# Optimization experiments

Measured on AMD Instinct MI355X. Metric: run time of the kernel, lower is better.

## Reference

```python
import jax, jax.numpy as jnp
import numpy as np


def setup_inputs() -> dict:
    key = jax.random.key(0)
    k1, k2 = jax.random.split(key)
    B, H, W = 8, 720, 1280
    input1 = jax.random.normal(k1, (B, 2, H, W), dtype=jnp.float32)   # flow (fx, fy)
    input2 = jax.random.uniform(k2, (B, 1, H, W), dtype=jnp.float32)  # depth weight > 0
    return {"input1": input1, "input2": input2}


def _depth_flow_projection(flow, depth):
    # flow:  [B, 2, H, W]; depth: [B, 1, H, W]
    # Faithful to DAIN's DepthFlowProjection CUDA kernel with fillhole=0
    # (requires_grad=True path): each source pixel splats -flow * depth to the
    # 4 integer neighbors of its projected location, count accumulates depth
    # at the same 4 neighbors, then output /= count where count > 0.
    B, _, H, W = flow.shape
    fx = flow[:, 0]           # [B, H, W]
    fy = flow[:, 1]
    d = depth[:, 0]

    jj = jnp.arange(W, dtype=flow.dtype)[None, None, :]
    ii = jnp.arange(H, dtype=flow.dtype)[None, :, None]
    x2 = jj + fx              # projected x, [B, H, W]
    y2 = ii + fy              # projected y

    valid = (x2 >= 0) & (x2 <= W - 1) & (y2 >= 0) & (y2 <= H - 1)
    w = jnp.where(valid, d, 0.0)  # zero weight kills out-of-bounds splats

    xL = jnp.clip(jnp.floor(x2), 0, W - 1).astype(jnp.int32)
    yT = jnp.clip(jnp.floor(y2), 0, H - 1).astype(jnp.int32)
    xR = jnp.minimum(xL + 1, W - 1)
    yB = jnp.minimum(yT + 1, H - 1)

    boff = (jnp.arange(B, dtype=jnp.int32) * (H * W))[:, None, None]
    # flat indices for the 4 corners, each [B*H*W]
    corners = [(yT, xL), (yT, xR), (yB, xL), (yB, xR)]
    idx = jnp.stack([(boff + yy * W + xx).reshape(-1) for yy, xx in corners], 0).reshape(-1)  # [4*B*H*W]

    def rep4(v):
        v = v.reshape(-1)
        return jnp.broadcast_to(v[None, :], (4, v.shape[0])).reshape(-1)

    N = B * H * W
    count = jnp.zeros((N,), flow.dtype).at[idx].add(rep4(w))
    ox = jnp.zeros((N,), flow.dtype).at[idx].add(rep4(-fx * w))
    oy = jnp.zeros((N,), flow.dtype).at[idx].add(rep4(-fy * w))

    has = count > 0
    denom = jnp.where(has, count, 1.0)
    ox = jnp.where(has, ox / denom, 0.0)
    oy = jnp.where(has, oy / denom, 0.0)
    return jnp.stack([ox.reshape(B, H, W), oy.reshape(B, H, W)], axis=1)  # [B, 2, H, W]


def reference(input1, input2):
    return _depth_flow_projection(input1, input2)
```

## Files before the change

### kernel.cpp

```cpp
#include <hip/hip_runtime.h>

constexpr int B  = 8;
constexpr int H  = 720;
constexpr int W  = 1280;
constexpr int HW = H * W;
constexpr int N  = B * HW;

constexpr int TX = 64;
constexpr int TY = 16;
constexpr int C  = 3;
constexpr int RW = TX + 2 * C;
constexpr int RH = TY + 2 * C;
constexpr int RN = RW * RH;
constexpr int PY = 4;

__global__ __launch_bounds__(256) void dfp_zero(float* __restrict__ p)
{
    size_t t = ((size_t)blockIdx.x * 256 + threadIdx.x) * 4;
    *(float4*)(p + t) = make_float4(0.f, 0.f, 0.f, 0.f);
}

__global__ __launch_bounds__(256) void dfp_outlier(
    const float* __restrict__ flow, const float* __restrict__ depth,
    float* __restrict__ pcnt, float* __restrict__ pox, float* __restrict__ poy)
{
    int t = blockIdx.x * 256 + threadIdx.x;
    if (t >= N / 4) return;
    int t4 = t * 4;
    int b  = t4 / HW;
    int p  = t4 - b * HW;
    int i  = p / W;
    int j  = p - i * W;

    const float* fxp = flow + b * 2 * HW;
    float4 fx4 = *(const float4*)(fxp + p);
    float4 fy4 = *(const float4*)(fxp + HW + p);
    float fxs[4] = {fx4.x, fx4.y, fx4.z, fx4.w};
    float fys[4] = {fy4.x, fy4.y, fy4.z, fy4.w};

    float* cb = pcnt + b * HW;
    float* xb = pox  + b * HW;
    float* yb = poy  + b * HW;

    #pragma unroll
    for (int e = 0; e < 4; ++e) {
        float fx = fxs[e], fy = fys[e];
        float x2 = (float)(j + e) + fx;
        float y2 = (float)i + fy;
        bool valid = (x2 >= 0.0f) && (x2 <= (float)(W - 1)) &&
                     (y2 >= 0.0f) && (y2 <= (float)(H - 1));
        bool band  = (fx >= -3.0f) && (fx < 3.0f) &&
                     (fy >= -3.0f) && (fy < 3.0f);
        bool fast  = band && (x2 < (float)(W - 1)) && (y2 < (float)(H - 1));
        if (valid && !fast) {
            float d  = depth[t4 + e];
            int xL = (int)floorf(x2);
            int yT = (int)floorf(y2);
            int xR = min(xL + 1, W - 1);
            int yB = min(yT + 1, H - 1);
            float w = d, gx = -fx * d, gy = -fy * d;
            int n00 = yT * W + xL, n01 = yT * W + xR;
            int n10 = yB * W + xL, n11 = yB * W + xR;
            unsafeAtomicAdd(&cb[n00], w); unsafeAtomicAdd(&xb[n00], gx); unsafeAtomicAdd(&yb[n00], gy);
            unsafeAtomicAdd(&cb[n01], w); unsafeAtomicAdd(&xb[n01], gx); unsafeAtomicAdd(&yb[n01], gy);
            unsafeAtomicAdd(&cb[n10], w); unsafeAtomicAdd(&xb[n10], gx); unsafeAtomicAdd(&yb[n10], gy);
            unsafeAtomicAdd(&cb[n11], w); unsafeAtomicAdd(&xb[n11], gx); unsafeAtomicAdd(&yb[n11], gy);
        }
    }
}

__global__ __launch_bounds__(256) void dfp_gather(
    const float* __restrict__ flow, const float* __restrict__ depth,
    const float* __restrict__ pcnt, const float* __restrict__ pox,
    const float* __restrict__ poy, float* __restrict__ out)
{
    __shared__ float4 sq[RN];

    const int tid = threadIdx.x;
    const int tx0 = blockIdx.x * TX;
    const int ty0 = blockIdx.y * TY;
    const int b   = blockIdx.z;

    const float* fxp = flow + b * 2 * HW;
    const float* fyp = fxp + HW;
    const float* dp  = depth + b * HW;

    for (int k = tid; k < RN; k += 256) {
        int ry = k / RW;
        int rx = k - ry * RW;
        int gy = ty0 - C + ry;
        int gx = tx0 - C + rx;
        float X = 0.f, Y = 0.f, w = 0.f;
        if ((unsigned)gy < (unsigned)H && (unsigned)gx < (unsigned)W) {
            int g = gy * W + gx;
            float fx = fxp[g];
            float fy = fyp[g];
            float x2 = (float)gx + fx;
            float y2 = (float)gy + fy;
            if (fx >= -3.0f && fx < 3.0f && fy >= -3.0f && fy < 3.0f &&
                x2 >= 0.0f && x2 < (float)(W - 1) &&
                y2 >= 0.0f && y2 < (float)(H - 1)) {
                X = x2; Y = y2; w = dp[g];
            }
        }
        sq[k] = make_float4(X, Y, w, 0.f);
    }
    __syncthreads();

    const int ox  = tid & 63;
    const int g0  = tid >> 6;
    const int oxa = tx0 + ox;

    const float oxaF = (float)oxa;
    const float cLo  = oxaF - 1.0f;
    const float cHi  = oxaF + 1.0f;

    const int oy0 = g0 * PY;
    const int oyb = ty0 + oy0;
    const float oybF = (float)oyb;
    const float bm1 = oybF - 1.0f;
    const float b0  = oybF;
    const float b1  = oybF + 1.0f;
    const float b2  = oybF + 2.0f;
    const float b3  = oybF + 3.0f;
    const float b4  = oybF + 4.0f;

    float c0 = 0.f, c1 = 0.f, c2 = 0.f, c3 = 0.f;
    float x0 = 0.f, x1 = 0.f, x2a = 0.f, x3 = 0.f;
    float y0 = 0.f, y1 = 0.f, y2a = 0.f, y3 = 0.f;

    for (int dy = -C; dy <= PY - 1 + C; ++dy) {
        const int   base = (oy0 + dy + C) * RW + ox;
        const float gyF  = oybF + (float)dy;
        #pragma unroll
        for (int dx = -C; dx <= C; ++dx) {
            float4 f = sq[base + dx + C];
            const float X = f.x, Y = f.y, w = f.z;
            bool cx  = (X >= cLo) & (X < cHi);
            bool tm1 = (Y >= bm1);
            bool t0  = (Y >= b0);
            bool t1  = (Y >= b1);
            bool t2  = (Y >= b2);
            bool t3  = (Y >= b3);
            bool t4  = (Y >= b4);
            bool m0 = cx & tm1 & !t1;
            bool m1 = cx & t0  & !t2;
            bool m2 = cx & t1  & !t3;
            bool m3 = cx & t2  & !t4;

            float ax = (oxaF + (float)dx) - X;
            float ay = gyF - Y;

            float w0 = m0 ? w : 0.0f;
            float w1 = m1 ? w : 0.0f;
            float w2 = m2 ? w : 0.0f;
            float w3 = m3 ? w : 0.0f;
            c0 += w0;  x0  = fmaf(ax, w0, x0 );  y0  = fmaf(ay, w0, y0 );
            c1 += w1;  x1  = fmaf(ax, w1, x1 );  y1  = fmaf(ay, w1, y1 );
            c2 += w2;  x2a = fmaf(ax, w2, x2a);  y2a = fmaf(ay, w2, y2a);
            c3 += w3;  x3  = fmaf(ax, w3, x3 );  y3  = fmaf(ay, w3, y3 );
        }
    }

    float* outx = out + b * 2 * HW;
    float* outy = outx + HW;
    const float* cb = pcnt + b * HW;
    const float* xb = pox  + b * HW;
    const float* yb = poy  + b * HW;

    float cc[PY] = {c0, c1, c2, c3};
    float vx[PY] = {x0, x1, x2a, x3};
    float vy[PY] = {y0, y1, y2a, y3};
    #pragma unroll
    for (int r = 0; r < PY; ++r) {
        int ga = (oyb + r) * W + oxa;
        float c  = cc[r] + cb[ga];
        float fx = vx[r] + xb[ga];
        float fy = vy[r] + yb[ga];
        bool has = c > 0.0f;
        outx[ga] = has ? fx / c : 0.0f;
        outy[ga] = has ? fy / c : 0.0f;
    }
}

__global__ __launch_bounds__(256) void dfp_scatter(
    const float* __restrict__ flow, const float* __restrict__ depth,
    float* __restrict__ out, float* __restrict__ count)
{
    int t = blockIdx.x * 256 + threadIdx.x;
    if (t >= N) return;
    int b = t / HW;
    int p = t - b * HW;
    int i = p / W;
    int j = p - i * W;
    const int fbase = b * 2 * HW;
    float fx = flow[fbase + p];
    float fy = flow[fbase + HW + p];
    float d  = depth[t];
    float x2 = (float)j + fx;
    float y2 = (float)i + fy;
    if (!(x2 >= 0.0f && x2 <= (float)(W - 1) &&
          y2 >= 0.0f && y2 <= (float)(H - 1))) return;
    int xL = (int)floorf(x2);
    int yT = (int)floorf(y2);
    int xR = min(xL + 1, W - 1);
    int yB = min(yT + 1, H - 1);
    float w = d, gx = -fx * w, gy = -fy * w;
    float* ox = out + fbase;
    float* oy = out + fbase + HW;
    float* cnt = count + b * HW;
    int n00 = yT * W + xL, n01 = yT * W + xR, n10 = yB * W + xL, n11 = yB * W + xR;
    unsafeAtomicAdd(&cnt[n00], w); unsafeAtomicAdd(&ox[n00], gx); unsafeAtomicAdd(&oy[n00], gy);
    unsafeAtomicAdd(&cnt[n01], w); unsafeAtomicAdd(&ox[n01], gx); unsafeAtomicAdd(&oy[n01], gy);
    unsafeAtomicAdd(&cnt[n10], w); unsafeAtomicAdd(&ox[n10], gx); unsafeAtomicAdd(&oy[n10], gy);
    unsafeAtomicAdd(&cnt[n11], w); unsafeAtomicAdd(&ox[n11], gx); unsafeAtomicAdd(&oy[n11], gy);
}

__global__ __launch_bounds__(256) void dfp_normalize(
    float* __restrict__ out, const float* __restrict__ count)
{
    int t = blockIdx.x * 256 + threadIdx.x;
    if (t >= N / 4) return;
    int t4 = t * 4;
    int b  = t4 / HW;
    int p  = t4 - b * HW;
    float4 c = *(const float4*)(count + t4);
    float* ox = out + b * 2 * HW + p;
    float* oy = ox + HW;
    float4 vx = *(const float4*)ox;
    float4 vy = *(const float4*)oy;
    vx.x = (c.x > 0.0f) ? vx.x / c.x : 0.0f;
    vx.y = (c.y > 0.0f) ? vx.y / c.y : 0.0f;
    vx.z = (c.z > 0.0f) ? vx.z / c.z : 0.0f;
    vx.w = (c.w > 0.0f) ? vx.w / c.w : 0.0f;
    vy.x = (c.x > 0.0f) ? vy.x / c.x : 0.0f;
    vy.y = (c.y > 0.0f) ? vy.y / c.y : 0.0f;
    vy.z = (c.z > 0.0f) ? vy.z / c.z : 0.0f;
    vy.w = (c.w > 0.0f) ? vy.w / c.w : 0.0f;
    *(float4*)ox = vx;
    *(float4*)oy = vy;
}

extern "C" void kernel_launch(void* const* d_in, const int* in_sizes, int n_in,
                              void* d_out, int out_size, void* d_ws, size_t ws_size,
                              hipStream_t stream)
{
    const float* flow  = (const float*)d_in[0];
    const float* depth = (const float*)d_in[1];
    float* out = (float*)d_out;

    if (ws_size >= (size_t)3 * N * sizeof(float)) {
        float* pcnt = (float*)d_ws;
        float* pox  = pcnt + N;
        float* poy  = pox + N;
        dfp_zero<<<(3 * N / 4) / 256, 256, 0, stream>>>(pcnt);
        dfp_outlier<<<(N / 4 + 255) / 256, 256, 0, stream>>>(flow, depth, pcnt, pox, poy);
        dim3 grid(W / TX, H / TY, B);
        dfp_gather<<<grid, 256, 0, stream>>>(flow, depth, pcnt, pox, poy, out);
    } else if (ws_size >= (size_t)N * sizeof(float)) {
        float* count = (float*)d_ws;
        hipMemsetAsync(out,   0, (size_t)2 * N * sizeof(float), stream);
        hipMemsetAsync(count, 0, (size_t)N * sizeof(float),     stream);
        dfp_scatter  <<<(N + 255) / 256,     256, 0, stream>>>(flow, depth, out, count);
        dfp_normalize<<<(N / 4 + 255) / 256, 256, 0, stream>>>(out, count);
    }
}
```

Before: 248.4 us.

## Register-block gather kernel to 2x3 outputs per thread with parity-split shared tile

The gather kernel now computes a 2-column by 3-row block of output pixels per thread instead of a 1x4 column strip, using a 128x12 tile. The shared tile is stored with even and odd columns split into separate halves, so each loaded candidate is reused across two output columns without bank conflicts. Final loads and stores become float2. The aim is fewer shared-memory loads per output and better amortized comparisons; the cost is more accumulator registers, hence the added occupancy hint in launch bounds.

Result: slower. 280.0 us (+12.7%).

```diff
diff --git a/kernel.cpp b/kernel.cpp
--- a/kernel.cpp
+++ b/kernel.cpp
@@ -6,13 +6,12 @@
 constexpr int HW = H * W;
 constexpr int N  = B * HW;
 
-constexpr int TX = 64;
-constexpr int TY = 16;
-constexpr int C  = 3;
-constexpr int RW = TX + 2 * C;
-constexpr int RH = TY + 2 * C;
-constexpr int RN = RW * RH;
-constexpr int PY = 4;
+constexpr int TX  = 128;
+constexpr int TY  = 12;
+constexpr int C   = 3;
+constexpr int RWS = TX + 2 * C;
+constexpr int RHS = TY + 2 * C;
+constexpr int RNS = RWS * RHS;
 
 __global__ __launch_bounds__(256) void dfp_zero(float* __restrict__ p)
 {
@@ -69,12 +68,12 @@
     }
 }
 
-__global__ __launch_bounds__(256) void dfp_gather(
+__global__ __launch_bounds__(256, 4) void dfp_gather(
     const float* __restrict__ flow, const float* __restrict__ depth,
     const float* __restrict__ pcnt, const float* __restrict__ pox,
     const float* __restrict__ poy, float* __restrict__ out)
 {
-    __shared__ float4 sq[RN];
+    __shared__ float4 sq[RNS];
 
     const int tid = threadIdx.x;
     const int tx0 = blockIdx.x * TX;
@@ -85,11 +84,11 @@
     const float* fyp = fxp + HW;
     const float* dp  = depth + b * HW;
 
-    for (int k = tid; k < RN; k += 256) {
-        int ry = k / RW;
-        int rx = k - ry * RW;
+    for (int k = tid; k < RNS; k += 256) {
+        int ry = k / RWS;
+        int s  = k - ry * RWS;
         int gy = ty0 - C + ry;
-        int gx = tx0 - C + rx;
+        int gx = tx0 - C + s;
         float X = 0.f, Y = 0.f, w = 0.f;
         if ((unsigned)gy < (unsigned)H && (unsigned)gx < (unsigned)W) {
             int g = gy * W + gx;
@@ -103,62 +102,77 @@
                 X = x2; Y = y2; w = dp[g];
             }
         }
-        sq[k] = make_float4(X, Y, w, 0.f);
+        int idx = ry * RWS + (s & 1) * (RWS / 2) + (s >> 1);
+        sq[idx] = make_float4(X, Y, w, 0.f);
     }
     __syncthreads();
 
-    const int ox  = tid & 63;
-    const int g0  = tid >> 6;
-    const int oxa = tx0 + ox;
-
-    const float oxaF = (float)oxa;
-    const float cLo  = oxaF - 1.0f;
-    const float cHi  = oxaF + 1.0f;
-
-    const int oy0 = g0 * PY;
-    const int oyb = ty0 + oy0;
+    const int cg   = tid & 63;
+    const int rg   = tid >> 6;
+    const int oxa0 = tx0 + 2 * cg;
+
+    const float oxaF = (float)oxa0;
+    const float cm1 = oxaF - 1.0f;
+    const float cc0 = oxaF;
+    const float cp1 = oxaF + 1.0f;
+    const float cp2 = oxaF + 2.0f;
+
+    const int oyb = ty0 + rg * 3;
     const float oybF = (float)oyb;
     const float bm1 = oybF - 1.0f;
-    const float b0  = oybF;
-    const float b1  = oybF + 1.0f;
-    const float b2  = oybF + 2.0f;
-    const float b3  = oybF + 3.0f;
-    const float b4  = oybF + 4.0f;
-
-    float c0 = 0.f, c1 = 0.f, c2 = 0.f, c3 = 0.f;
-    float x0 = 0.f, x1 = 0.f, x2a = 0.f, x3 = 0.f;
-    float y0 = 0.f, y1 = 0.f, y2a = 0.f, y3 = 0.f;
-
-    for (int dy = -C; dy <= PY - 1 + C; ++dy) {
-        const int   base = (oy0 + dy + C) * RW + ox;
-        const float gyF  = oybF + (float)dy;
+    const float b0_ = oybF;
+    const float b1_ = oybF + 1.0f;
+    const float b2_ = oybF + 2.0f;
+    const float b3_ = oybF + 3.0f;
+
+    float c00=0.f,c01=0.f,c02=0.f, c10=0.f,c11=0.f,c12=0.f;
+    float x00=0.f,x01=0.f,x02=0.f, x10=0.f,x11=0.f,x12=0.f;
+    float y00=0.f,y01=0.f,y02=0.f, y10=0.f,y11=0.f,y12=0.f;
+
+    for (int dy = -C; dy <= 2 + C; ++dy) {
+        const int   rb  = (rg * 3 + dy + C) * RWS;
+        const int   be  = rb + cg;
+        const int   bo  = rb + (RWS / 2) + cg;
+        const float gyF = oybF + (float)dy;
+
         #pragma unroll
-        for (int dx = -C; dx <= C; ++dx) {
-            float4 f = sq[base + dx + C];
-            const float X = f.x, Y = f.y, w = f.z;
-            bool cx  = (X >= cLo) & (X < cHi);
-            bool tm1 = (Y >= bm1);
-            bool t0  = (Y >= b0);
-            bool t1  = (Y >= b1);
-            bool t2  = (Y >= b2);
-            bool t3  = (Y >= b3);
-            bool t4  = (Y >= b4);
-            bool m0 = cx & tm1 & !t1;
-            bool m1 = cx & t0  & !t2;
-            bool m2 = cx & t1  & !t3;
-            bool m3 = cx & t2  & !t4;
-
-            float ax = (oxaF + (float)dx) - X;
-            float ay = gyF - Y;
-
-            float w0 = m0 ? w : 0.0f;
-            float w1 = m1 ? w : 0.0f;
-            float w2 = m2 ? w : 0.0f;
-            float w3 = m3 ? w : 0.0f;
-            c0 += w0;  x0  = fmaf(ax, w0, x0 );  y0  = fmaf(ay, w0, y0 );
-            c1 += w1;  x1  = fmaf(ax, w1, x1 );  y1  = fmaf(ay, w1, y1 );
-            c2 += w2;  x2a = fmaf(ax, w2, x2a);  y2a = fmaf(ay, w2, y2a);
-            c3 += w3;  x3  = fmaf(ax, w3, x3 );  y3  = fmaf(ay, w3, y3 );
+        for (int j = 0; j < 4; ++j) {
+            float4 fe = sq[be + j];
+            float4 fo = sq[bo + j];
+
+            #pragma unroll
+            for (int pcand = 0; pcand < 2; ++pcand) {
+                float4 f   = pcand ? fo : fe;
+                float  gxF = oxaF + (float)(2 * j - 3 + pcand);
+                const float X = f.x, Y = f.y, w = f.z;
+
+                bool vm1 = (X >= cm1), v0 = (X >= cc0);
+                bool v1  = (X >= cp1), v2 = (X >= cp2);
+                bool um1 = (Y >= bm1), u0 = (Y >= b0_);
+                bool u1  = (Y >= b1_), u2 = (Y >= b2_), u3 = (Y >= b3_);
+                bool mc0 = vm1 & !v1;
+                bool mc1 = v0  & !v2;
+                bool mr0 = um1 & !u1;
+                bool mr1 = u0  & !u2;
+                bool mr2 = u1  & !u3;
+
+                float ax = gxF - X;
+                float ay = gyF - Y;
+
+                float w00 = (mc0 & mr0) ? w : 0.0f;
+                float w01 = (mc0 & mr1) ? w : 0.0f;
+                float w02 = (mc0 & mr2) ? w : 0.0f;
+                float w10 = (mc1 & mr0) ? w : 0.0f;
+                float w11 = (mc1 & mr1) ? w : 0.0f;
+                float w12 = (mc1 & mr2) ? w : 0.0f;
+
+                c00 += w00; x00 = fmaf(ax, w00, x00); y00 = fmaf(ay, w00, y00);
+                c01 += w01; x01 = fmaf(ax, w01, x01); y01 = fmaf(ay, w01, y01);
+                c02 += w02; x02 = fmaf(ax, w02, x02); y02 = fmaf(ay, w02, y02);
+                c10 += w10; x10 = fmaf(ax, w10, x10); y10 = fmaf(ay, w10, y10);
+                c11 += w11; x11 = fmaf(ax, w11, x11); y11 = fmaf(ay, w11, y11);
+                c12 += w12; x12 = fmaf(ax, w12, x12); y12 = fmaf(ay, w12, y12);
+            }
         }
     }
 
@@ -168,18 +182,31 @@
     const float* xb = pox  + b * HW;
     const float* yb = poy  + b * HW;
 
-    float cc[PY] = {c0, c1, c2, c3};
-    float vx[PY] = {x0, x1, x2a, x3};
-    float vy[PY] = {y0, y1, y2a, y3};
+    float cA[3] = {c00, c01, c02};
+    float cB[3] = {c10, c11, c12};
+    float xA[3] = {x00, x01, x02};
+    float xB[3] = {x10, x11, x12};
+    float yA[3] = {y00, y01, y02};
+    float yB[3] = {y10, y11, y12};
+
     #pragma unroll
-    for (int r = 0; r < PY; ++r) {
-        int ga = (oyb + r) * W + oxa;
-        float c  = cc[r] + cb[ga];
-        float fx = vx[r] + xb[ga];
-        float fy = vy[r] + yb[ga];
-        bool has = c > 0.0f;
-        outx[ga] = has ? fx / c : 0.0f;
-        outy[ga] = has ? fy / c : 0.0f;
+    for (int r = 0; r < 3; ++r) {
+        int ga = (oyb + r) * W + oxa0;
+        float2 c2 = *(const float2*)(cb + ga);
+        float2 xv = *(const float2*)(xb + ga);
+        float2 yv = *(const float2*)(yb + ga);
+        float ca = cA[r] + c2.x;
+        float cbv = cB[r] + c2.y;
+        float fxa = xA[r] + xv.x;
+        float fxb = xB[r] + xv.y;
+        float fya = yA[r] + yv.x;
+        float fyb = yB[r] + yv.y;
+        bool hA = ca  > 0.0f;
+        bool hB = cbv > 0.0f;
+        float2 ox2 = make_float2(hA ? fxa / ca : 0.0f, hB ? fxb / cbv : 0.0f);
+        float2 oy2 = make_float2(hA ? fya / ca : 0.0f, hB ? fyb / cbv : 0.0f);
+        *(float2*)(outx + ga) = ox2;
+        *(float2*)(outy + ga) = oy2;
     }
 }
 
```
